# Optimization experiments

Measured on AMD Instinct MI355X. Metric: run time of the kernel, lower is better.

Reference implementation:

```python
import jax, jax.numpy as jnp
import numpy as np

D_MODEL = 512
NHEAD = 8
COORD_DIM = 3
B, N = 2, 2048


def setup_inputs() -> dict:
    key = jax.random.key(0)
    ks = jax.random.split(key, 6)
    x = jax.random.normal(ks[0], (B, N, D_MODEL), dtype=jnp.float32)
    coords = jax.random.normal(ks[1], (B, N, COORD_DIM), dtype=jnp.float32)
    attn_mask = jax.random.normal(ks[2], (N, N), dtype=jnp.float32)
    # qkv Linear(d_model, 3*d_model) with bias
    lim = 1.0 / np.sqrt(D_MODEL)
    qkv_w = jax.random.uniform(ks[3], (3 * D_MODEL, D_MODEL), dtype=jnp.float32, minval=-lim, maxval=lim)
    qkv_b = jax.random.uniform(ks[4], (3 * D_MODEL,), dtype=jnp.float32, minval=-lim, maxval=lim)
    # rel_weight is zeros-init in torch; use small random values for a nontrivial test
    rel_weight = 0.02 * jax.random.normal(ks[5], (NHEAD, COORD_DIM), dtype=jnp.float32)
    return {"x": x, "coords": coords, "attn_mask": attn_mask,
            "qkv_w": qkv_w, "qkv_b": qkv_b, "rel_weight": rel_weight}


def reference(x, coords, attn_mask, qkv_w, qkv_b, rel_weight):
    Bb, Nn, D = x.shape
    H = rel_weight.shape[0]
    hd = D // H
    scale = 1.0 / jnp.sqrt(jnp.asarray(hd, dtype=x.dtype))

    qkv = x @ qkv_w.T + qkv_b                      # [B,N,3D]
    q, k, v = jnp.split(qkv, 3, axis=-1)

    def to_heads(t):
        return t.reshape(Bb, Nn, H, hd).transpose(0, 2, 1, 3)  # [B,H,N,hd]

    qh, kh, vh = to_heads(q), to_heads(k), to_heads(v)

    # per-head scalar projection of coordinates: [B,H,N]
    coord_proj = jnp.einsum('bnc,hc->bhn', coords.astype(jnp.float32), rel_weight).astype(x.dtype)

    # scores with relative-coordinate bias and additive float mask (2d kind)
    scores = jnp.einsum('bhqd,bhkd->bhqk', qh, kh) * scale
    scores = scores + coord_proj[:, :, :, None] - coord_proj[:, :, None, :]
    scores = scores + attn_mask[None, None, :, :]

    attn = jax.nn.softmax(scores, axis=-1)
    yh = jnp.einsum('bhqk,bhkd->bhqd', attn, vh)   # [B,H,N,hd]
    return yh.transpose(0, 2, 1, 3).reshape(Bb, Nn, D)
```

## Files before the change

kernel.cpp:

```cpp
#include <hip/hip_runtime.h>
#include <hip/hip_bf16.h>

typedef __bf16 bf16;
typedef __bf16 bf16x4 __attribute__((ext_vector_type(4)));
typedef __bf16 bf16x8 __attribute__((ext_vector_type(8)));
typedef float floatx4 __attribute__((ext_vector_type(4)));

#define D_MODEL 512
#define NHEAD 8
#define HD 64
#define NB 2
#define NN 2048
#define BH (NB*NHEAD)

__global__ __launch_bounds__(256) void convxw(const float* __restrict__ x,
                                              const float* __restrict__ w,
                                              bf16* __restrict__ xb,
                                              bf16* __restrict__ wb) {
    int idx = blockIdx.x * 256 + threadIdx.x;
    const float* src; bf16* dst; int i4;
    if (idx < 524288) { src = x; dst = xb; i4 = idx; }
    else              { src = w; dst = wb; i4 = idx - 524288; }
    float4 v = *(const float4*)(src + (size_t)i4*4);
    bf16x4 o; o[0] = (bf16)v.x; o[1] = (bf16)v.y; o[2] = (bf16)v.z; o[3] = (bf16)v.w;
    *(bf16x4*)(dst + (size_t)i4*4) = o;
}

__global__ __launch_bounds__(256) void coordproj(const float* __restrict__ coords,
                                                 const float* __restrict__ rw,
                                                 float* __restrict__ cp) {
    int idx = blockIdx.x * 256 + threadIdx.x;
    int b = idx >> 11, n = idx & 2047;
    float c0 = coords[idx*3 + 0];
    float c1 = coords[idx*3 + 1];
    float c2 = coords[idx*3 + 2];
    for (int h = 0; h < NHEAD; h++) {
        float v = c0*rw[h*3+0] + c1*rw[h*3+1] + c2*rw[h*3+2];
        cp[(size_t)(b*NHEAD + h)*NN + n] = v;
    }
}

__global__ __launch_bounds__(256, 4) void qkv_gemm(const bf16* __restrict__ xb,
                                                   const bf16* __restrict__ wb,
                                                   const float* __restrict__ bias,
                                                   bf16* __restrict__ qb,
                                                   bf16* __restrict__ kb,
                                                   bf16* __restrict__ vtb) {
    __shared__ bf16 smem[64*72 + 128*72];
    bf16 (*Ws)[72] = (bf16(*)[72])smem;
    bf16 (*Xs)[72] = (bf16(*)[72])(smem + 64*72);
    int t = threadIdx.x;
    int w = t >> 6, lane = t & 63, quad = lane >> 4, l15 = lane & 15;
    int blk = blockIdx.x;
    int bf = blk % 24, bm = blk / 24;
    int f0 = bf * 64, m0 = bm * 128;

    floatx4 acc[4][2] = {};
    int wrow = t >> 2, wcol = (t & 3) * 16;
    int xrow = t >> 1, xcol = (t & 1) * 32;

    for (int k0 = 0; k0 < D_MODEL; k0 += 64) {
        __syncthreads();
        {
            const bf16* wsrc = wb + (size_t)(f0 + wrow)*D_MODEL + k0 + wcol;
            *(bf16x8*)&Ws[wrow][wcol]   = *(const bf16x8*)wsrc;
            *(bf16x8*)&Ws[wrow][wcol+8] = *(const bf16x8*)(wsrc + 8);
            const bf16* xsrc = xb + (size_t)(m0 + xrow)*D_MODEL + k0 + xcol;
            *(bf16x8*)&Xs[xrow][xcol]    = *(const bf16x8*)xsrc;
            *(bf16x8*)&Xs[xrow][xcol+8]  = *(const bf16x8*)(xsrc + 8);
            *(bf16x8*)&Xs[xrow][xcol+16] = *(const bf16x8*)(xsrc + 16);
            *(bf16x8*)&Xs[xrow][xcol+24] = *(const bf16x8*)(xsrc + 24);
        }
        __syncthreads();
        for (int kf = 0; kf < 2; kf++) {
            bf16x8 af[4], bx[2];
            for (int fi = 0; fi < 4; fi++)
                af[fi] = *(const bf16x8*)&Ws[fi*16 + l15][kf*32 + quad*8];
            for (int mj = 0; mj < 2; mj++)
                bx[mj] = *(const bf16x8*)&Xs[w*32 + mj*16 + l15][kf*32 + quad*8];
            for (int fi = 0; fi < 4; fi++)
                for (int mj = 0; mj < 2; mj++)
                    acc[fi][mj] = __builtin_amdgcn_mfma_f32_16x16x32_bf16(af[fi], bx[mj], acc[fi][mj], 0, 0, 0);
        }
    }

    int mat = f0 >> 9;
    int h = (f0 >> 6) & 7;
    int b = m0 >> 11;
    int nb = m0 & 2047;
    size_t bho = (size_t)(b*NHEAD + h);
    float4 bs4[4];
    for (int fi = 0; fi < 4; fi++)
        bs4[fi] = *(const float4*)(bias + f0 + fi*16 + quad*4);

    if (mat < 2) {
        bf16* dst = (mat == 0) ? qb : kb;
        float sc = (mat == 0) ? 0.125f : 1.0f;
        for (int fi = 0; fi < 4; fi++) {
            for (int mj = 0; mj < 2; mj++) {
                int n = nb + w*32 + mj*16 + l15;
                bf16x4 pv;
                pv[0] = (bf16)((acc[fi][mj][0] + bs4[fi].x) * sc);
                pv[1] = (bf16)((acc[fi][mj][1] + bs4[fi].y) * sc);
                pv[2] = (bf16)((acc[fi][mj][2] + bs4[fi].z) * sc);
                pv[3] = (bf16)((acc[fi][mj][3] + bs4[fi].w) * sc);
                *(bf16x4*)(dst + (bho*NN + n)*HD + fi*16 + quad*4) = pv;
            }
        }
    } else {
        __syncthreads();
        bf16* Vt = smem;
        for (int fi = 0; fi < 4; fi++) {
            int d = fi*16 + quad*4;
            for (int mj = 0; mj < 2; mj++) {
                int mlc = w*32 + mj*16 + l15;
                Vt[(d+0)*136 + mlc] = (bf16)(acc[fi][mj][0] + bs4[fi].x);
                Vt[(d+1)*136 + mlc] = (bf16)(acc[fi][mj][1] + bs4[fi].y);
                Vt[(d+2)*136 + mlc] = (bf16)(acc[fi][mj][2] + bs4[fi].z);
                Vt[(d+3)*136 + mlc] = (bf16)(acc[fi][mj][3] + bs4[fi].w);
            }
        }
        __syncthreads();
        int d = t >> 2, mc = (t & 3) * 32;
        bf16* gdst = vtb + (bho*HD + d)*NN + nb + mc;
        for (int c = 0; c < 4; c++)
            *(bf16x8*)(gdst + c*8) = *(const bf16x8*)&Vt[d*136 + mc + c*8];
    }
}

__global__ __launch_bounds__(256, 4) void attn(const bf16* __restrict__ qb,
                                               const bf16* __restrict__ kb,
                                               const bf16* __restrict__ vtb,
                                               const float* __restrict__ maskf,
                                               const float* __restrict__ cp,
                                               float* __restrict__ op,
                                               float* __restrict__ ml,
                                               float* __restrict__ out,
                                               int ksplit) {
    __shared__ bf16 Ks[64][72];
    __shared__ bf16 Vts[64][72];
    __shared__ bf16 Ps[64][72];
    __shared__ float Cs[2048];
    int t = threadIdx.x;
    int w = t >> 6, lane = t & 63;
    int quad = lane >> 4, l15 = lane & 15;
    int blk = blockIdx.x;
    int bh = blk & 15;
    int rest = blk >> 4;
    int qt = rest & 31, kp = rest >> 5;
    int q0 = qt * 64;
    int nkeys = NN / ksplit;
    int ntiles = nkeys / 64;
    int kbase = kp * nkeys;
    size_t bhoff = (size_t)bh * (NN * HD);

    bf16x8 aq0, aq1;
    {
        const bf16* qp = qb + bhoff + (size_t)(q0 + w*16 + l15)*HD + quad*8;
        aq0 = *(const bf16x8*)(qp);
        aq1 = *(const bf16x8*)(qp + 32);
    }

    float m_i = -1e30f, l_i = 0.f;
    floatx4 o[4] = {};
    int qrow = q0 + w*16 + l15;
    const float* mrow = maskf + (size_t)qrow * NN;
    const float* cpb = cp + (size_t)bh * NN;
    int srow = t >> 2, scol = (t & 3) * 16;

    for (int i = t; i < nkeys; i += 256) Cs[i] = cpb[kbase + i];
    __syncthreads();

    bf16x8 kr0, kr1, vr0, vr1;
    float4 bias4[4];
    {
        const bf16* ks = kb + bhoff + (size_t)(kbase + srow)*HD + scol;
        kr0 = *(const bf16x8*)ks; kr1 = *(const bf16x8*)(ks + 8);
        const bf16* vs = vtb + bhoff + (size_t)srow*NN + kbase + scol;
        vr0 = *(const bf16x8*)vs; vr1 = *(const bf16x8*)(vs + 8);
        for (int j = 0; j < 4; j++) {
            float4 mv = *(const float4*)(mrow + kbase + j*16 + quad*4);
            float4 cv = *(const float4*)&Cs[j*16 + quad*4];
            bias4[j].x = mv.x - cv.x; bias4[j].y = mv.y - cv.y;
            bias4[j].z = mv.z - cv.z; bias4[j].w = mv.w - cv.w;
        }
    }

    for (int kt = 0; kt < ntiles; kt++) {
        __syncthreads();
        *(bf16x8*)&Ks[srow][scol]      = kr0;
        *(bf16x8*)&Ks[srow][scol + 8]  = kr1;
        *(bf16x8*)&Vts[srow][scol]     = vr0;
        *(bf16x8*)&Vts[srow][scol + 8] = vr1;
        __syncthreads();

        float4 mn4[4];
        bool more = (kt + 1 < ntiles);
        if (more) {
            int kn = kbase + (kt+1)*64;
            const bf16* ks = kb + bhoff + (size_t)(kn + srow)*HD + scol;
            kr0 = *(const bf16x8*)ks; kr1 = *(const bf16x8*)(ks + 8);
            const bf16* vs = vtb + bhoff + (size_t)srow*NN + kn + scol;
            vr0 = *(const bf16x8*)vs; vr1 = *(const bf16x8*)(vs + 8);
            for (int j = 0; j < 4; j++)
                mn4[j] = *(const float4*)(mrow + kn + j*16 + quad*4);
        }

        floatx4 s[4];
        for (int j = 0; j < 4; j++) {
            s[j][0] = bias4[j].x; s[j][1] = bias4[j].y;
            s[j][2] = bias4[j].z; s[j][3] = bias4[j].w;
            bf16x8 ka0 = *(const bf16x8*)&Ks[j*16 + l15][quad*8];
            bf16x8 ka1 = *(const bf16x8*)&Ks[j*16 + l15][32 + quad*8];
            s[j] = __builtin_amdgcn_mfma_f32_16x16x32_bf16(ka0, aq0, s[j], 0, 0, 0);
            s[j] = __builtin_amdgcn_mfma_f32_16x16x32_bf16(ka1, aq1, s[j], 0, 0, 0);
        }

        float mx = s[0][0];
        for (int j = 0; j < 4; j++)
            for (int r = 0; r < 4; r++) mx = fmaxf(mx, s[j][r]);
        mx = fmaxf(mx, __shfl_xor(mx, 16));
        mx = fmaxf(mx, __shfl_xor(mx, 32));
        float mnew = fmaxf(m_i, mx);
        float al = __expf(m_i - mnew);
        float rs = 0.f;
        for (int j = 0; j < 4; j++)
            for (int r = 0; r < 4; r++) {
                float p = __expf(s[j][r] - mnew);
                s[j][r] = p;
                rs += p;
            }
        rs += __shfl_xor(rs, 16);
        rs += __shfl_xor(rs, 32);
        l_i = l_i * al + rs;
        m_i = mnew;

        float alc[4];
        for (int r = 0; r < 4; r++) alc[r] = __shfl(al, quad*4 + r);
        for (int dj = 0; dj < 4; dj++)
            for (int r = 0; r < 4; r++) o[dj][r] *= alc[r];

        for (int j = 0; j < 4; j++) {
            bf16x4 pv;
            pv[0] = (bf16)s[j][0]; pv[1] = (bf16)s[j][1];
            pv[2] = (bf16)s[j][2]; pv[3] = (bf16)s[j][3];
            *(bf16x4*)&Ps[w*16 + l15][j*16 + quad*4] = pv;
        }

        for (int kf2 = 0; kf2 < 2; kf2++) {
            bf16x8 ap = *(const bf16x8*)&Ps[w*16 + l15][kf2*32 + quad*8];
            for (int dj = 0; dj < 4; dj++) {
                bf16x8 bv = *(const bf16x8*)&Vts[dj*16 + l15][kf2*32 + quad*8];
                o[dj] = __builtin_amdgcn_mfma_f32_16x16x32_bf16(ap, bv, o[dj], 0, 0, 0);
            }
        }

        if (more) {
            int kn_loc = (kt+1)*64;
            for (int j = 0; j < 4; j++) {
                float4 cv = *(const float4*)&Cs[kn_loc + j*16 + quad*4];
                bias4[j].x = mn4[j].x - cv.x; bias4[j].y = mn4[j].y - cv.y;
                bias4[j].z = mn4[j].z - cv.z; bias4[j].w = mn4[j].w - cv.w;
            }
        }
    }

    int b = bh >> 3, h = bh & 7;
    if (ksplit == 1) {
        float lc[4];
        for (int r = 0; r < 4; r++) lc[r] = __shfl(l_i, quad*4 + r);
        for (int dj = 0; dj < 4; dj++) {
            for (int r = 0; r < 4; r++) {
                int n = q0 + w*16 + quad*4 + r;
                out[((size_t)(b*NN + n))*D_MODEL + h*HD + dj*16 + l15] = o[dj][r] / lc[r];
            }
        }
    } else {
        size_t pbase = (size_t)kp * BH * NN;
        for (int dj = 0; dj < 4; dj++) {
            for (int r = 0; r < 4; r++) {
                int n = q0 + w*16 + quad*4 + r;
                op[(pbase + bh*NN + n)*HD + dj*16 + l15] = o[dj][r];
            }
        }
        if (quad == 0) {
            float2 v; v.x = m_i; v.y = l_i;
            *(float2*)(ml + (pbase + (size_t)bh*NN + qrow)*2) = v;
        }
    }
}

__global__ __launch_bounds__(256) void combineN(const float* __restrict__ op,
                                                const float* __restrict__ ml,
                                                float* __restrict__ out,
                                                int ksplit) {
    int idx = blockIdx.x * 256 + threadIdx.x;
    int row = idx >> 4, c4 = (idx & 15) * 4;
    float mstar = -1e30f;
    for (int kp = 0; kp < ksplit; kp++)
        mstar = fmaxf(mstar, ml[((size_t)kp*BH*NN + row)*2]);
    float denom = 0.f;
    float ax = 0.f, ay = 0.f, az = 0.f, aw = 0.f;
    for (int kp = 0; kp < ksplit; kp++) {
        float2 m2 = *(const float2*)(ml + ((size_t)kp*BH*NN + row)*2);
        float wgt = __expf(m2.x - mstar);
        denom += wgt * m2.y;
        float4 ov = *(const float4*)(op + ((size_t)kp*BH*NN + row)*HD + c4);
        ax += wgt*ov.x; ay += wgt*ov.y; az += wgt*ov.z; aw += wgt*ov.w;
    }
    float inv = 1.0f / denom;
    int bh = row >> 11, q = row & 2047;
    int b = bh >> 3, h = bh & 7;
    float4 res; res.x = ax*inv; res.y = ay*inv; res.z = az*inv; res.w = aw*inv;
    *(float4*)(out + ((size_t)(b*NN + q))*D_MODEL + h*HD + c4) = res;
}

extern "C" void kernel_launch(void* const* d_in, const int* in_sizes, int n_in,
                              void* d_out, int out_size, void* d_ws, size_t ws_size,
                              hipStream_t stream) {
    const float* x      = (const float*)d_in[0];
    const float* coords = (const float*)d_in[1];
    const float* amask  = (const float*)d_in[2];
    const float* qkv_w  = (const float*)d_in[3];
    const float* qkv_b  = (const float*)d_in[4];
    const float* rw     = (const float*)d_in[5];
    float* out = (float*)d_out;

    char* ws = (char*)d_ws;
    float* cp  = (float*)(ws + 0);
    bf16*  xb  = (bf16*) (ws + 131072);
    bf16*  wb  = (bf16*) (ws + 4325376);
    bf16*  qb  = (bf16*) (ws + 5898240);
    bf16*  kb  = (bf16*) (ws + 10092544);
    bf16*  vtb = (bf16*) (ws + 14286848);
    float* op  = (float*)(ws + 18481152);

    int split = 1;
    if (ws_size >= 53084160u)      split = 4;
    else if (ws_size >= 35782656u) split = 2;
    float* ml = (float*)(ws + 18481152 + (size_t)split*8388608);

    convxw   <<<dim3(2816), dim3(256), 0, stream>>>(x, qkv_w, xb, wb);
    coordproj<<<dim3(16),   dim3(256), 0, stream>>>(coords, rw, cp);
    qkv_gemm <<<dim3(768),  dim3(256), 0, stream>>>(xb, wb, qkv_b, qb, kb, vtb);
    attn     <<<dim3(512*split), dim3(256), 0, stream>>>(qb, kb, vtb, amask, cp, op, ml, out, split);
    if (split > 1)
        combineN<<<dim3(2048), dim3(256), 0, stream>>>(op, ml, out, split);
}
```

Before: 152.5 us.

## Fuse coord projection into conversion kernel, use exp2 softmax, drop LDS coord staging

Merges the coordinate-projection kernel into the fp32-to-bf16 conversion kernel, removing one launch. Folds log2(e) into the Q scale, the coordinate projection and the mask bias so the softmax can use the hardware exp2 instruction directly. Removes the shared-memory staging of the coordinate bias and its barrier, reading it from global memory instead, and changes the P tile padding to 68 with split 4-element LDS reads. This shrinks LDS use (possibly raising occupancy) and cuts exp cost, at the risk of more global loads and different bank-conflict behaviour on the P reads.

```diff
diff --git a/kernel.cpp b/kernel.cpp
--- a/kernel.cpp
+++ b/kernel.cpp
@@ -12,32 +12,35 @@
 #define NB 2
 #define NN 2048
 #define BH (NB*NHEAD)
+#define LOG2E 1.4426950408889634f
 
 __global__ __launch_bounds__(256) void convxw(const float* __restrict__ x,
                                               const float* __restrict__ w,
+                                              const float* __restrict__ coords,
+                                              const float* __restrict__ rw,
                                               bf16* __restrict__ xb,
-                                              bf16* __restrict__ wb) {
-    int idx = blockIdx.x * 256 + threadIdx.x;
+                                              bf16* __restrict__ wb,
+                                              float* __restrict__ cp) {
+    int bid = blockIdx.x;
+    if (bid >= 2816) {
+        int idx = (bid - 2816) * 256 + threadIdx.x;
+        int b = idx >> 11, n = idx & 2047;
+        float c0 = coords[idx*3 + 0];
+        float c1 = coords[idx*3 + 1];
+        float c2 = coords[idx*3 + 2];
+        for (int h = 0; h < NHEAD; h++) {
+            float v = c0*rw[h*3+0] + c1*rw[h*3+1] + c2*rw[h*3+2];
+            cp[(size_t)(b*NHEAD + h)*NN + n] = v * LOG2E;
+        }
+        return;
+    }
+    int idx = bid * 256 + threadIdx.x;
     const float* src; bf16* dst; int i4;
     if (idx < 524288) { src = x; dst = xb; i4 = idx; }
     else              { src = w; dst = wb; i4 = idx - 524288; }
     float4 v = *(const float4*)(src + (size_t)i4*4);
     bf16x4 o; o[0] = (bf16)v.x; o[1] = (bf16)v.y; o[2] = (bf16)v.z; o[3] = (bf16)v.w;
     *(bf16x4*)(dst + (size_t)i4*4) = o;
-}
-
-__global__ __launch_bounds__(256) void coordproj(const float* __restrict__ coords,
-                                                 const float* __restrict__ rw,
-                                                 float* __restrict__ cp) {
-    int idx = blockIdx.x * 256 + threadIdx.x;
-    int b = idx >> 11, n = idx & 2047;
-    float c0 = coords[idx*3 + 0];
-    float c1 = coords[idx*3 + 1];
-    float c2 = coords[idx*3 + 2];
-    for (int h = 0; h < NHEAD; h++) {
-        float v = c0*rw[h*3+0] + c1*rw[h*3+1] + c2*rw[h*3+2];
-        cp[(size_t)(b*NHEAD + h)*NN + n] = v;
-    }
 }
 
 __global__ __launch_bounds__(256, 4) void qkv_gemm(const bf16* __restrict__ xb,
@@ -95,7 +98,7 @@
 
     if (mat < 2) {
         bf16* dst = (mat == 0) ? qb : kb;
-        float sc = (mat == 0) ? 0.125f : 1.0f;
+        float sc = (mat == 0) ? 0.125f * LOG2E : 1.0f;
         for (int fi = 0; fi < 4; fi++) {
             for (int mj = 0; mj < 2; mj++) {
                 int n = nb + w*32 + mj*16 + l15;
@@ -139,8 +142,7 @@
                                                int ksplit) {
     __shared__ bf16 Ks[64][72];
     __shared__ bf16 Vts[64][72];
-    __shared__ bf16 Ps[64][72];
-    __shared__ float Cs[2048];
+    __shared__ bf16 Ps[64][68];
     int t = threadIdx.x;
     int w = t >> 6, lane = t & 63;
     int quad = lane >> 4, l15 = lane & 15;
@@ -165,11 +167,8 @@
     floatx4 o[4] = {};
     int qrow = q0 + w*16 + l15;
     const float* mrow = maskf + (size_t)qrow * NN;
-    const float* cpb = cp + (size_t)bh * NN;
+    const float* cpb = cp + (size_t)bh * NN + kbase;
     int srow = t >> 2, scol = (t & 3) * 16;
-
-    for (int i = t; i < nkeys; i += 256) Cs[i] = cpb[kbase + i];
-    __syncthreads();
 
     bf16x8 kr0, kr1, vr0, vr1;
     float4 bias4[4];
@@ -180,9 +179,11 @@
         vr0 = *(const bf16x8*)vs; vr1 = *(const bf16x8*)(vs + 8);
         for (int j = 0; j < 4; j++) {
             float4 mv = *(const float4*)(mrow + kbase + j*16 + quad*4);
-            float4 cv = *(const float4*)&Cs[j*16 + quad*4];
-            bias4[j].x = mv.x - cv.x; bias4[j].y = mv.y - cv.y;
-            bias4[j].z = mv.z - cv.z; bias4[j].w = mv.w - cv.w;
+            float4 cv = *(const float4*)(cpb + j*16 + quad*4);
+            bias4[j].x = fmaf(mv.x, LOG2E, -cv.x);
+            bias4[j].y = fmaf(mv.y, LOG2E, -cv.y);
+            bias4[j].z = fmaf(mv.z, LOG2E, -cv.z);
+            bias4[j].w = fmaf(mv.w, LOG2E, -cv.w);
         }
     }
 
@@ -222,11 +223,11 @@
         mx = fmaxf(mx, __shfl_xor(mx, 16));
         mx = fmaxf(mx, __shfl_xor(mx, 32));
         float mnew = fmaxf(m_i, mx);
-        float al = __expf(m_i - mnew);
+        float al = __builtin_amdgcn_exp2f(m_i - mnew);
         float rs = 0.f;
         for (int j = 0; j < 4; j++)
             for (int r = 0; r < 4; r++) {
-                float p = __expf(s[j][r] - mnew);
+                float p = __builtin_amdgcn_exp2f(s[j][r] - mnew);
                 s[j][r] = p;
                 rs += p;
             }
@@ -248,7 +249,11 @@
         }
 
         for (int kf2 = 0; kf2 < 2; kf2++) {
-            bf16x8 ap = *(const bf16x8*)&Ps[w*16 + l15][kf2*32 + quad*8];
+            bf16x4 apl = *(const bf16x4*)&Ps[w*16 + l15][kf2*32 + quad*8];
+            bf16x4 aph = *(const bf16x4*)&Ps[w*16 + l15][kf2*32 + quad*8 + 4];
+            bf16x8 ap;
+            ap[0]=apl[0]; ap[1]=apl[1]; ap[2]=apl[2]; ap[3]=apl[3];
+            ap[4]=aph[0]; ap[5]=aph[1]; ap[6]=aph[2]; ap[7]=aph[3];
             for (int dj = 0; dj < 4; dj++) {
                 bf16x8 bv = *(const bf16x8*)&Vts[dj*16 + l15][kf2*32 + quad*8];
                 o[dj] = __builtin_amdgcn_mfma_f32_16x16x32_bf16(ap, bv, o[dj], 0, 0, 0);
@@ -258,9 +263,11 @@
         if (more) {
             int kn_loc = (kt+1)*64;
             for (int j = 0; j < 4; j++) {
-                float4 cv = *(const float4*)&Cs[kn_loc + j*16 + quad*4];
-                bias4[j].x = mn4[j].x - cv.x; bias4[j].y = mn4[j].y - cv.y;
-                bias4[j].z = mn4[j].z - cv.z; bias4[j].w = mn4[j].w - cv.w;
+                float4 cv = *(const float4*)(cpb + kn_loc + j*16 + quad*4);
+                bias4[j].x = fmaf(mn4[j].x, LOG2E, -cv.x);
+                bias4[j].y = fmaf(mn4[j].y, LOG2E, -cv.y);
+                bias4[j].z = fmaf(mn4[j].z, LOG2E, -cv.z);
+                bias4[j].w = fmaf(mn4[j].w, LOG2E, -cv.w);
             }
         }
     }
@@ -303,7 +310,7 @@
     float ax = 0.f, ay = 0.f, az = 0.f, aw = 0.f;
     for (int kp = 0; kp < ksplit; kp++) {
         float2 m2 = *(const float2*)(ml + ((size_t)kp*BH*NN + row)*2);
-        float wgt = __expf(m2.x - mstar);
+        float wgt = __builtin_amdgcn_exp2f(m2.x - mstar);
         denom += wgt * m2.y;
         float4 ov = *(const float4*)(op + ((size_t)kp*BH*NN + row)*HD + c4);
         ax += wgt*ov.x; ay += wgt*ov.y; az += wgt*ov.z; aw += wgt*ov.w;
@@ -340,8 +347,7 @@
     else if (ws_size >= 35782656u) split = 2;
     float* ml = (float*)(ws + 18481152 + (size_t)split*8388608);
 
-    convxw   <<<dim3(2816), dim3(256), 0, stream>>>(x, qkv_w, xb, wb);
-    coordproj<<<dim3(16),   dim3(256), 0, stream>>>(coords, rw, cp);
+    convxw   <<<dim3(2832), dim3(256), 0, stream>>>(x, qkv_w, coords, rw, xb, wb, cp);
     qkv_gemm <<<dim3(768),  dim3(256), 0, stream>>>(xb, wb, qkv_b, qb, kb, vtb);
     attn     <<<dim3(512*split), dim3(256), 0, stream>>>(qb, kb, vtb, amask, cp, op, ml, out, split);
     if (split > 1)
```

Result: slower. 155.7 us (+2.1%).
